# Kernel tuning notes

Hardware: AMD Instinct MI355X
Metric: run time of the kernel (lower is better)

## Reference

```python
import jax, jax.numpy as jnp
import numpy as np

D = 1024

def setup_inputs() -> dict:
    key = jax.random.key(0)
    ks = jax.random.split(key, 9)
    B, S = 4, 2048
    s = 1.0 / np.sqrt(D)
    return {
        "query": jax.random.normal(ks[0], (B, S, D), jnp.float32),
        "key": jax.random.normal(ks[1], (B, S, D), jnp.float32),
        "value": jax.random.normal(ks[2], (B, S, D), jnp.float32),
        "Wq": jax.random.normal(ks[3], (D, D), jnp.float32) * s,
        "bq": jax.random.normal(ks[4], (D,), jnp.float32) * 0.01,
        "Wk": jax.random.normal(ks[5], (D, D), jnp.float32) * s,
        "bk": jax.random.normal(ks[6], (D,), jnp.float32) * 0.01,
        "Wv": jax.random.normal(ks[7], (D, D), jnp.float32) * s,
        "bv": jax.random.normal(ks[8], (D,), jnp.float32) * 0.01,
    }

def reference(query, key, value, Wq, bq, Wk, bk, Wv, bv):
    scale = 1.0 / (query.shape[-1] ** 0.5)
    q = jnp.einsum('bsd,ed->bse', query, Wq) + bq  # nn.Linear: x @ W.T + b
    k = jnp.einsum('bsd,ed->bse', key, Wk) + bk
    v = jnp.einsum('bsd,ed->bse', value, Wv) + bv
    scores = jnp.einsum('bqd,bkd->bqk', q, k) * scale  # [B, Sq, Skv]
    w = jax.nn.softmax(scores, axis=-1)
    return jnp.einsum('bqk,bkd->bqd', w, v)
```

## Files before the change

kernel.cpp:

```cpp
#include <hip/hip_runtime.h>

typedef __bf16 bf16x8 __attribute__((ext_vector_type(8)));
typedef float f32x4 __attribute__((ext_vector_type(4)));
typedef unsigned short u16x8 __attribute__((ext_vector_type(8)));

__device__ inline unsigned short f2bf(float f) {
  union { float f; unsigned u; } a; a.f = f;
  return (unsigned short)((a.u + 0x7fffu + ((a.u >> 16) & 1u)) >> 16);
}
__device__ inline float bf2f(unsigned short h) {
  union { unsigned u; float f; } a; a.u = ((unsigned)h) << 16;
  return a.f;
}

__global__ __launch_bounds__(256) void cvtW(const float* __restrict__ Wq,
                                            const float* __restrict__ Wk,
                                            const float* __restrict__ Wv,
                                            unsigned short* __restrict__ Wb) {
  int i = blockIdx.x * 256 + threadIdx.x;
  int idx = i >> 18;
  int off = i & 262143;
  const float* s = (idx == 0) ? Wq : ((idx == 1) ? Wk : Wv);
  float4 v = ((const float4*)s)[off];
  ushort4 o;
  o.x = f2bf(v.x); o.y = f2bf(v.y); o.z = f2bf(v.z); o.w = f2bf(v.w);
  ((ushort4*)(Wb + idx * 1048576))[off] = o;
}

#define G2L(gp, lp) __builtin_amdgcn_global_load_lds( \
    (const __attribute__((address_space(1))) void*)(gp), \
    (__attribute__((address_space(3))) void*)(lp), 16, 0, 0)

#define MFMA_(d, a, b) d = __builtin_amdgcn_mfma_f32_16x16x32_bf16(a, b, d, 0, 0, 0)
#define SB0() __builtin_amdgcn_sched_barrier(0)
#define LGKM(n) do { asm volatile("s_waitcnt lgkmcnt(" #n ")" ::: "memory"); SB0(); } while (0)
#define VMC(n) do { asm volatile("s_waitcnt vmcnt(" #n ")" ::: "memory"); SB0(); } while (0)

struct PJ {
  const float* A0; const float* A1; const float* A2;
  const unsigned short* B;
  unsigned short* outQ; unsigned short* outK; unsigned short* outV;
  const float* biasQ; const float* biasK; const float* biasV;
};

__global__ __launch_bounds__(512, 2) void gemmP(PJ p) {
  extern __shared__ char smem[];
  char* smA = smem;
  char* smB = smem + 65536;
  const int tid = threadIdx.x, lane = tid & 63, wid = tid >> 6;
  const int wm = wid >> 1, wn = wid & 1;

  int orig = blockIdx.x + 8 * (blockIdx.y + 32 * blockIdx.z);
  int wg = (orig & 7) * 96 + (orig >> 3);
  int bx = wg & 7; int t2 = wg >> 3; int by = t2 & 31; int z = t2 >> 5;
  const int m0 = by << 8, n0 = bx << 7;

  const float* Az = (z == 0) ? p.A0 : ((z == 1) ? p.A1 : p.A2);

  const int lineT = tid >> 3;
  const int sg = (tid & 7) ^ (lineT & 7);
  const char* srcA = (const char*)(Az + (long long)(m0 + lineT) * 1024) + (sg << 4);
  const int srowB = 2 * lineT + (sg >> 2);
  const char* srcB = (const char*)(p.B + (long long)z * 1048576
                                   + (long long)(n0 + srowB) * 1024) + ((sg & 3) << 4);

  const int aBase = (((wm << 6) + (lane & 15)) << 7);
  const int ax = lane & 7;
  const int ck0 = ((((lane >> 4) << 1) | 0) ^ ax) << 4;
  const int ck1 = ((((lane >> 4) << 1) | 1) ^ ax) << 4;
  const int rb2 = (lane & 15) >> 1;
  const int bBase = ((wn << 5) + rb2) << 7;
  const int bX = ((((lane & 1) << 2) | (lane >> 4)) ^ rb2) << 4;

  f32x4 acc[4][4];
#pragma unroll
  for (int i = 0; i < 4; ++i)
#pragma unroll
    for (int j = 0; j < 4; ++j) acc[i][j] = (f32x4){0.f, 0.f, 0.f, 0.f};

  f32x4 aLoF[2][2], aHiF[2][2];
  bf16x8 aLoB[2], aHiB[2], bLo[2], bHi[2];

  auto stage = [&](int t) {
    char* dA = smA + ((t & 1) << 15) + (tid << 4);
    char* dB = smB + ((t & 1) << 13) + (tid << 4);
    const char* sA = srcA + (long long)t * 128;
#pragma unroll
    for (int c = 0; c < 4; ++c) G2L(sA + ((long long)c << 18), dA + (c << 13));
    G2L(srcB + (long long)t * 64, dB);
  };
  auto readA = [&](int b, int half, f32x4 (&dst)[2][2]) {
    const char* ra = smA + (b << 15) + aBase + (half << 12);
#pragma unroll
    for (int f = 0; f < 2; ++f) {
      dst[f][0] = *(const f32x4*)(ra + (f << 11) + ck0);
      dst[f][1] = *(const f32x4*)(ra + (f << 11) + ck1);
    }
  };
  auto readB = [&](int b, int half, bf16x8 (&dst)[2]) {
    const char* rb = smB + (b << 13) + bBase + (half << 11);
#pragma unroll
    for (int f = 0; f < 2; ++f)
      dst[f] = *(const bf16x8*)(rb + (f << 10) + bX);
  };
  auto cvtA = [&](f32x4 (&s)[2][2], bf16x8 (&d)[2]) {
#pragma unroll
    for (int f = 0; f < 2; ++f)
      d[f] = (bf16x8){(__bf16)s[f][0][0], (__bf16)s[f][0][1],
                      (__bf16)s[f][0][2], (__bf16)s[f][0][3],
                      (__bf16)s[f][1][0], (__bf16)s[f][1][1],
                      (__bf16)s[f][1][2], (__bf16)s[f][1][3]};
  };
  auto quadP = [&](int qa, int qb, bf16x8 (&A)[2], bf16x8 (&B)[2]) {
    __builtin_amdgcn_s_setprio(1);
#pragma unroll
    for (int mi = 0; mi < 2; ++mi)
#pragma unroll
      for (int ni = 0; ni < 2; ++ni)
        MFMA_(acc[qa * 2 + mi][qb * 2 + ni], A[mi], B[ni]);
    __builtin_amdgcn_s_setprio(0);
  };

  stage(0);
  VMC(0);
  __builtin_amdgcn_s_barrier();
  readA(0, 0, aLoF); readB(0, 0, bLo);
  SB0();

  const int NT = 32;
  for (int t = 0; t < NT; ++t) {
    if (t + 1 < NT) stage(t + 1);
    SB0();
    LGKM(2);
    cvtA(aLoF, aLoB);
    readA(t & 1, 1, aHiF);
    SB0();
    LGKM(4);
    quadP(0, 0, aLoB, bLo);
    readB(t & 1, 1, bHi);
    SB0();
    LGKM(2);
    cvtA(aHiF, aHiB);
    quadP(1, 0, aHiB, bLo);
    LGKM(0);
    quadP(0, 1, aLoB, bHi);
    quadP(1, 1, aHiB, bHi);
    VMC(0);
    __builtin_amdgcn_s_barrier();
    if (t + 1 < NT) { readA((t + 1) & 1, 0, aLoF); readB((t + 1) & 1, 0, bLo); }
    SB0();
  }

  const int c0 = lane & 15, r0 = (lane >> 4) << 2;
  if (z < 2) {
    unsigned short* O = (z == 0) ? p.outQ : p.outK;
    const float* bias = (z == 0) ? p.biasQ : p.biasK;
#pragma unroll
    for (int mi = 0; mi < 4; ++mi) {
      const int grow = m0 + (wm << 6) + (mi << 4) + r0;
#pragma unroll
      for (int ni = 0; ni < 4; ++ni) {
        const int gcol = n0 + (wn << 6) + (ni << 4) + c0;
        const float bb = bias[gcol];
#pragma unroll
        for (int rr = 0; rr < 4; ++rr)
          O[(long long)(grow + rr) * 1024 + gcol] = f2bf(acc[mi][ni][rr] + bb);
      }
    }
  } else {
#pragma unroll
    for (int mi = 0; mi < 4; ++mi) {
      const int grow = m0 + (wm << 6) + (mi << 4) + r0;
      const int bb = grow >> 11, s = grow & 2047;
#pragma unroll
      for (int ni = 0; ni < 4; ++ni) {
        const int d = n0 + (wn << 6) + (ni << 4) + c0;
        const float ba = p.biasV[d];
        ushort4 pk;
        pk.x = f2bf(acc[mi][ni][0] + ba);
        pk.y = f2bf(acc[mi][ni][1] + ba);
        pk.z = f2bf(acc[mi][ni][2] + ba);
        pk.w = f2bf(acc[mi][ni][3] + ba);
        *(ushort4*)(p.outV + ((long long)bb << 21) + (long long)d * 2048 + s) = pk;
      }
    }
  }
}

#define EPI_SCALE 1
#define EPI_OUT 2

struct GP {
  const unsigned short* A;
  const unsigned short* B;
  unsigned short* C;
  long long batchA, batchB, batchC;
  int lda, ldb, ldc, K;
  float scale;
};

template<int BM, int BN, int WMW, int WNW, int EPI>
__global__ __launch_bounds__(512, 2) void gemm2(GP p) {
  constexpr int NWN = BN / WNW;
  constexpr int AMF = WMW / 16, BNF = WNW / 16;
  constexpr int AH = AMF / 2, BH = BNF / 2;
  constexpr int AF_N = AH * 2;
  constexpr int NBA = BM / 64, NBB = BN / 64;
  static_assert((BM / WMW) * NWN == 8, "8 waves");
  static_assert(BNF == 4, "lgkm immediates assume BNF==4");

  extern __shared__ char smem[];
  char* smA = smem;
  char* smB = smem + 2 * BM * 128;

  const int tid = threadIdx.x;
  const int lane = tid & 63;
  const int wid = tid >> 6;
  const int wm = wid / NWN, wn = wid % NWN;

  const int gx = gridDim.x, gy = gridDim.y;
  const int nwg = gx * gy * (int)gridDim.z;
  int orig = blockIdx.x + gx * (blockIdx.y + gy * blockIdx.z);
  int qq = nwg >> 3, rr_ = nwg & 7;
  int xcd = orig & 7, sl = orig >> 3;
  int wg = (xcd < rr_ ? xcd * (qq + 1) : rr_ * (qq + 1) + (xcd - rr_) * qq) + sl;
  int bx = wg % gx;
  int t2 = wg / gx;
  int by = t2 % gy;
  int z  = t2 / gy;

  const int m0 = by * BM, n0 = bx * BN;

  const long long lda2 = (long long)p.lda * 2;
  const long long ldb2 = (long long)p.ldb * 2;
  const char* Abase = (const char*)(p.A + (long long)z * p.batchA) + (long long)m0 * lda2;
  const char* Bbase = (const char*)(p.B + (long long)z * p.batchB) + (long long)n0 * ldb2;

  const int trow = tid >> 3;
  const int cs = (((tid & 7) ^ (trow & 7)) << 4);
  const char* srcA = Abase + (long long)trow * lda2 + cs;
  const char* srcB = Bbase + (long long)trow * ldb2 + cs;

  const int NT = p.K >> 6;

  const int aRowB = ((wm * WMW + (lane & 15)) << 7);
  const int bRowB = ((wn * WNW + (lane & 15)) << 7);
  const int csw = (lane & 7) << 4;
  const int ck0 = (((lane >> 4) << 4)) ^ csw;
  const int ck1 = ((((lane >> 4) << 4)) | 64) ^ csw;

  f32x4 acc[AMF][BNF];
#pragma unroll
  for (int i = 0; i < AMF; ++i)
#pragma unroll
    for (int j = 0; j < BNF; ++j) acc[i][j] = (f32x4){0.f, 0.f, 0.f, 0.f};

  bf16x8 aLo[AH][2], aHi[AH][2], bLo[BH][2], bHi[BH][2];

  auto stage = [&](int t) {
    char* dA = smA + (t & 1) * (BM * 128) + (tid << 4);
    char* dB = smB + (t & 1) * (BN * 128) + (tid << 4);
    const char* sA = srcA + (long long)t * 128;
    const char* sB = srcB + (long long)t * 128;
#pragma unroll
    for (int c = 0; c < NBA; ++c) G2L(sA + (long long)c * (lda2 << 6), dA + c * 8192);
#pragma unroll
    for (int c = 0; c < NBB; ++c) G2L(sB + (long long)c * (ldb2 << 6), dB + c * 8192);
  };
  auto readAh = [&](int t, int half, bf16x8 (&dst)[AH][2]) {
    const char* ra = smA + (t & 1) * (BM * 128) + aRowB + half * (AH * 2048);
#pragma unroll
    for (int mi = 0; mi < AH; ++mi) {
      dst[mi][0] = *(const bf16x8*)(ra + mi * 2048 + ck0);
      dst[mi][1] = *(const bf16x8*)(ra + mi * 2048 + ck1);
    }
  };
  auto readBh = [&](int t, int half, bf16x8 (&dst)[BH][2]) {
    const char* rb = smB + (t & 1) * (BN * 128) + bRowB + half * (BH * 2048);
#pragma unroll
    for (int ni = 0; ni < BH; ++ni) {
      dst[ni][0] = *(const bf16x8*)(rb + ni * 2048 + ck0);
      dst[ni][1] = *(const bf16x8*)(rb + ni * 2048 + ck1);
    }
  };
  auto quad = [&](int qa, int qb, bf16x8 (&A)[AH][2], bf16x8 (&B)[BH][2]) {
    __builtin_amdgcn_s_setprio(1);
#pragma unroll
    for (int mi = 0; mi < AH; ++mi)
#pragma unroll
      for (int ni = 0; ni < BH; ++ni) {
        MFMA_(acc[qa * AH + mi][qb * BH + ni], A[mi][0], B[ni][0]);
        MFMA_(acc[qa * AH + mi][qb * BH + ni], A[mi][1], B[ni][1]);
      }
    __builtin_amdgcn_s_setprio(0);
  };

  stage(0); stage(1);
  if constexpr (NBA + NBB == 8) VMC(8); else VMC(6);
  __builtin_amdgcn_s_barrier();
  readAh(0, 0, aLo); readBh(0, 0, bLo);
  SB0();

  for (int t = 0; t < NT; ++t) {
    readAh(t, 1, aHi);
    SB0();
    if constexpr (AF_N == 8) LGKM(8); else LGKM(4);
    quad(0, 0, aLo, bLo);
    readBh(t, 1, bHi);
    SB0();
    LGKM(4);
    quad(1, 0, aHi, bLo);
    LGKM(0);
    quad(0, 1, aLo, bHi);
    quad(1, 1, aHi, bHi);
    VMC(0);
    __builtin_amdgcn_s_barrier();
    if (t + 2 < NT) stage(t + 2);
    if (t + 1 < NT) { readAh(t + 1, 0, aLo); readBh(t + 1, 0, bLo); }
    SB0();
  }

  const int c0 = lane & 15;
  const int r0 = (lane >> 4) << 2;
  if constexpr (EPI == EPI_SCALE) {
    unsigned short* Cz = p.C + (long long)z * p.batchC;
#pragma unroll
    for (int mi = 0; mi < AMF; ++mi) {
      const int grow = m0 + wm * WMW + (mi << 4) + r0;
#pragma unroll
      for (int ni = 0; ni < BNF; ++ni) {
        const int gcol = n0 + wn * WNW + (ni << 4) + c0;
#pragma unroll
        for (int rr = 0; rr < 4; ++rr)
          Cz[(long long)(grow + rr) * p.ldc + gcol] = f2bf(acc[mi][ni][rr] * p.scale);
      }
    }
  } else {
    float* Cz = (float*)p.C + (long long)z * p.batchC;
#pragma unroll
    for (int mi = 0; mi < AMF; ++mi) {
      const int grow = m0 + wm * WMW + (mi << 4) + r0;
#pragma unroll
      for (int ni = 0; ni < BNF; ++ni) {
        const int gcol = n0 + wn * WNW + (ni << 4) + c0;
#pragma unroll
        for (int rr = 0; rr < 4; ++rr)
          Cz[(long long)(grow + rr) * p.ldc + gcol] = acc[mi][ni][rr] * p.scale;
      }
    }
  }
}

__global__ __launch_bounds__(256) void softmax_rows(unsigned short* __restrict__ S) {
  const size_t row = blockIdx.x;
  unsigned short* pp = S + row * 2048;
  const int t = threadIdx.x, lane = t & 63, wave = t >> 6;
  u16x8 h = ((const u16x8*)pp)[t];
  float x[8];
#pragma unroll
  for (int j = 0; j < 8; ++j) x[j] = bf2f(h[j]);
  float m = x[0];
#pragma unroll
  for (int j = 1; j < 8; ++j) m = fmaxf(m, x[j]);
#pragma unroll
  for (int off = 32; off >= 1; off >>= 1) m = fmaxf(m, __shfl_xor(m, off, 64));
  __shared__ float rmax[4], rsum[4];
  if (lane == 0) rmax[wave] = m;
  __syncthreads();
  m = fmaxf(fmaxf(rmax[0], rmax[1]), fmaxf(rmax[2], rmax[3]));
  float e[8], sum = 0.f;
#pragma unroll
  for (int j = 0; j < 8; ++j) { e[j] = __expf(x[j] - m); sum += e[j]; }
#pragma unroll
  for (int off = 32; off >= 1; off >>= 1) sum += __shfl_xor(sum, off, 64);
  if (lane == 0) rsum[wave] = sum;
  __syncthreads();
  sum = rsum[0] + rsum[1] + rsum[2] + rsum[3];
  const float inv = 1.f / sum;
  u16x8 o;
#pragma unroll
  for (int j = 0; j < 8; ++j) o[j] = f2bf(e[j] * inv);
  ((u16x8*)pp)[t] = o;
}

extern "C" void kernel_launch(void* const* d_in, const int* in_sizes, int n_in,
                              void* d_out, int out_size, void* d_ws, size_t ws_size,
                              hipStream_t stream) {
  const float* q  = (const float*)d_in[0];
  const float* k  = (const float*)d_in[1];
  const float* v  = (const float*)d_in[2];
  const float* Wq = (const float*)d_in[3];
  const float* bq = (const float*)d_in[4];
  const float* Wk = (const float*)d_in[5];
  const float* bk = (const float*)d_in[6];
  const float* Wv = (const float*)d_in[7];
  const float* bv = (const float*)d_in[8];

  unsigned short* S  = (unsigned short*)d_ws;
  unsigned short* Wb = S + 16777216;
  unsigned short* qb = Wb + 3145728;
  unsigned short* kb = qb + 8388608;
  unsigned short* vT = kb + 8388608;

  (void)hipFuncSetAttribute((const void*)gemmP,
      hipFuncAttributeMaxDynamicSharedMemorySize, 81920);
  (void)hipFuncSetAttribute((const void*)gemm2<256,256,128,64,EPI_SCALE>,
      hipFuncAttributeMaxDynamicSharedMemorySize, 131072);
  (void)hipFuncSetAttribute((const void*)gemm2<256,128,64,64,EPI_OUT>,
      hipFuncAttributeMaxDynamicSharedMemorySize, 98304);

  cvtW<<<3072, 256, 0, stream>>>(Wq, Wk, Wv, Wb);

  PJ pj{};
  pj.A0 = q; pj.A1 = k; pj.A2 = v;
  pj.B = Wb;
  pj.outQ = qb; pj.outK = kb; pj.outV = vT;
  pj.biasQ = bq; pj.biasK = bk; pj.biasV = bv;
  gemmP<<<dim3(8, 32, 3), 512, 81920, stream>>>(pj);

  GP gs{};
  gs.A = qb; gs.batchA = 2097152; gs.lda = 1024;
  gs.B = kb; gs.batchB = 2097152; gs.ldb = 1024;
  gs.C = S;  gs.batchC = 4194304; gs.ldc = 2048;
  gs.K = 1024; gs.scale = 0.03125f;
  gemm2<256,256,128,64,EPI_SCALE><<<dim3(8, 8, 4), 512, 131072, stream>>>(gs);

  softmax_rows<<<8192, 256, 0, stream>>>(S);

  GP gv{};
  gv.A = S;  gv.batchA = 4194304; gv.lda = 2048;
  gv.B = vT; gv.batchB = 2097152; gv.ldb = 2048;
  gv.C = (unsigned short*)d_out; gv.batchC = 2097152; gv.ldc = 1024;
  gv.K = 2048; gv.scale = 1.f;
  gemm2<256,128,64,64,EPI_OUT><<<dim3(8, 8, 4), 512, 98304, stream>>>(gv);
}
```

Baseline: 166.9 us.

## Use 4-wave blocks with 64x128 per-wave tiles in projection GEMM

The QKV projection GEMM now runs with 256 threads (4 waves) instead of 512. Each wave covers a full 64x128 output slab, holding a 4x8 accumulator array instead of 4x4. The global-to-LDS staging, the swizzled LDS read addressing and the wait counts are rewritten to match. The aim is more MFMA work per LDS-loaded B fragment and fewer waves to synchronise, at the cost of higher register pressure and fewer waves to hide latency.

```diff
diff --git a/kernel.cpp b/kernel.cpp
--- a/kernel.cpp
+++ b/kernel.cpp
@@ -43,12 +43,12 @@
   const float* biasQ; const float* biasK; const float* biasV;
 };
 
-__global__ __launch_bounds__(512, 2) void gemmP(PJ p) {
+__global__ __launch_bounds__(256, 2) void gemmP(PJ p) {
   extern __shared__ char smem[];
   char* smA = smem;
   char* smB = smem + 65536;
   const int tid = threadIdx.x, lane = tid & 63, wid = tid >> 6;
-  const int wm = wid >> 1, wn = wid & 1;
+  const int wm = wid;
 
   int orig = blockIdx.x + 8 * (blockIdx.y + 32 * blockIdx.z);
   int wg = (orig & 7) * 96 + (orig >> 3);
@@ -57,51 +57,59 @@
 
   const float* Az = (z == 0) ? p.A0 : ((z == 1) ? p.A1 : p.A2);
 
-  const int lineT = tid >> 3;
-  const int sg = (tid & 7) ^ (lineT & 7);
-  const char* srcA = (const char*)(Az + (long long)(m0 + lineT) * 1024) + (sg << 4);
-  const int srowB = 2 * lineT + (sg >> 2);
-  const char* srcB = (const char*)(p.B + (long long)z * 1048576
-                                   + (long long)(n0 + srowB) * 1024) + ((sg & 3) << 4);
-
-  const int aBase = (((wm << 6) + (lane & 15)) << 7);
-  const int ax = lane & 7;
-  const int ck0 = ((((lane >> 4) << 1) | 0) ^ ax) << 4;
-  const int ck1 = ((((lane >> 4) << 1) | 1) ^ ax) << 4;
-  const int rb2 = (lane & 15) >> 1;
-  const int bBase = ((wn << 5) + rb2) << 7;
-  const int bX = ((((lane & 1) << 2) | (lane >> 4)) ^ rb2) << 4;
-
-  f32x4 acc[4][4];
+  const int sgA = (tid & 7) ^ ((tid >> 3) & 7);
+  const char* srcA = (const char*)Az
+      + ((long long)m0 + 2 * (tid >> 3) + (sgA >> 2)) * 4096 + ((sgA & 3) << 4);
+  const char* srcB = (const char*)(p.B + (long long)z * 1048576)
+      + ((long long)n0 + 2 * (tid >> 3) + (sgA >> 2)) * 2048 + ((sgA & 3) << 4);
+
+  const int kh = lane >> 4;
+  const int Ra0 = (wm << 6) + (lane & 15);
+  const int aJ = (kh >> 1) << 14;
+  const int kq0 = (kh & 1) << 1;
+  const int Rb0 = lane & 15;
+
+  f32x4 acc[4][8];
 #pragma unroll
   for (int i = 0; i < 4; ++i)
 #pragma unroll
-    for (int j = 0; j < 4; ++j) acc[i][j] = (f32x4){0.f, 0.f, 0.f, 0.f};
+    for (int j = 0; j < 8; ++j) acc[i][j] = (f32x4){0.f, 0.f, 0.f, 0.f};
 
   f32x4 aLoF[2][2], aHiF[2][2];
-  bf16x8 aLoB[2], aHiB[2], bLo[2], bHi[2];
+  bf16x8 aLoB[2], aHiB[2], bLo[4], bHi[4];
 
   auto stage = [&](int t) {
     char* dA = smA + ((t & 1) << 15) + (tid << 4);
     char* dB = smB + ((t & 1) << 13) + (tid << 4);
     const char* sA = srcA + (long long)t * 128;
-#pragma unroll
-    for (int c = 0; c < 4; ++c) G2L(sA + ((long long)c << 18), dA + (c << 13));
-    G2L(srcB + (long long)t * 64, dB);
+    const char* sB = srcB + (long long)t * 64;
+#pragma unroll
+    for (int c = 0; c < 8; ++c)
+      G2L(sA + (long long)(c & 3) * 64 * 4096 + ((c >> 2) << 6), dA + (c << 12));
+#pragma unroll
+    for (int c = 0; c < 2; ++c)
+      G2L(sB + (long long)c * 64 * 2048, dB + (c << 12));
   };
   auto readA = [&](int b, int half, f32x4 (&dst)[2][2]) {
-    const char* ra = smA + (b << 15) + aBase + (half << 12);
+    const char* ra = smA + (b << 15) + aJ;
 #pragma unroll
     for (int f = 0; f < 2; ++f) {
-      dst[f][0] = *(const f32x4*)(ra + (f << 11) + ck0);
-      dst[f][1] = *(const f32x4*)(ra + (f << 11) + ck1);
-    }
-  };
-  auto readB = [&](int b, int half, bf16x8 (&dst)[2]) {
-    const char* rb = smB + (b << 13) + bBase + (half << 11);
-#pragma unroll
-    for (int f = 0; f < 2; ++f)
-      dst[f] = *(const bf16x8*)(rb + (f << 10) + bX);
+      const int R = Ra0 + ((half * 2 + f) << 4);
+      const int lineB = (R >> 1) << 7;
+      const int x = ((R & 1) << 2) ^ ((R >> 1) & 7);
+      dst[f][0] = *(const f32x4*)(ra + lineB + ((x ^ (kq0 | 0)) << 4));
+      dst[f][1] = *(const f32x4*)(ra + lineB + ((x ^ (kq0 | 1)) << 4));
+    }
+  };
+  auto readB = [&](int b, int half, bf16x8 (&dst)[4]) {
+    const char* rb = smB + (b << 13);
+#pragma unroll
+    for (int f = 0; f < 4; ++f) {
+      const int R = Rb0 + ((half * 4 + f) << 4);
+      const int byte = ((R >> 1) << 7)
+                     + (((((R & 1) << 2) | kh) ^ ((R >> 1) & 7)) << 4);
+      dst[f] = *(const bf16x8*)(rb + byte);
+    }
   };
   auto cvtA = [&](f32x4 (&s)[2][2], bf16x8 (&d)[2]) {
 #pragma unroll
@@ -111,13 +119,13 @@
                       (__bf16)s[f][1][0], (__bf16)s[f][1][1],
                       (__bf16)s[f][1][2], (__bf16)s[f][1][3]};
   };
-  auto quadP = [&](int qa, int qb, bf16x8 (&A)[2], bf16x8 (&B)[2]) {
+  auto quadP = [&](int qa, int qb, bf16x8 (&A)[2], bf16x8 (&B)[4]) {
     __builtin_amdgcn_s_setprio(1);
 #pragma unroll
     for (int mi = 0; mi < 2; ++mi)
 #pragma unroll
-      for (int ni = 0; ni < 2; ++ni)
-        MFMA_(acc[qa * 2 + mi][qb * 2 + ni], A[mi], B[ni]);
+      for (int ni = 0; ni < 4; ++ni)
+        MFMA_(acc[qa * 2 + mi][qb * 4 + ni], A[mi], B[ni]);
     __builtin_amdgcn_s_setprio(0);
   };
 
@@ -130,16 +138,14 @@
   const int NT = 32;
   for (int t = 0; t < NT; ++t) {
     if (t + 1 < NT) stage(t + 1);
-    SB0();
-    LGKM(2);
+    readA(t & 1, 1, aHiF);
+    SB0();
+    LGKM(4);
     cvtA(aLoF, aLoB);
-    readA(t & 1, 1, aHiF);
-    SB0();
-    LGKM(4);
     quadP(0, 0, aLoB, bLo);
     readB(t & 1, 1, bHi);
     SB0();
-    LGKM(2);
+    LGKM(4);
     cvtA(aHiF, aHiB);
     quadP(1, 0, aHiB, bLo);
     LGKM(0);
@@ -159,8 +165,8 @@
     for (int mi = 0; mi < 4; ++mi) {
       const int grow = m0 + (wm << 6) + (mi << 4) + r0;
 #pragma unroll
-      for (int ni = 0; ni < 4; ++ni) {
-        const int gcol = n0 + (wn << 6) + (ni << 4) + c0;
+      for (int ni = 0; ni < 8; ++ni) {
+        const int gcol = n0 + (ni << 4) + c0;
         const float bb = bias[gcol];
 #pragma unroll
         for (int rr = 0; rr < 4; ++rr)
@@ -173,8 +179,8 @@
       const int grow = m0 + (wm << 6) + (mi << 4) + r0;
       const int bb = grow >> 11, s = grow & 2047;
 #pragma unroll
-      for (int ni = 0; ni < 4; ++ni) {
-        const int d = n0 + (wn << 6) + (ni << 4) + c0;
+      for (int ni = 0; ni < 8; ++ni) {
+        const int d = n0 + (ni << 4) + c0;
         const float ba = p.biasV[d];
         ushort4 pk;
         pk.x = f2bf(acc[mi][ni][0] + ba);
@@ -416,7 +422,7 @@
   pj.B = Wb;
   pj.outQ = qb; pj.outK = kb; pj.outV = vT;
   pj.biasQ = bq; pj.biasK = bk; pj.biasV = bv;
-  gemmP<<<dim3(8, 32, 3), 512, 81920, stream>>>(pj);
+  gemmP<<<dim3(8, 32, 3), 256, 81920, stream>>>(pj);
 
   GP gs{};
   gs.A = qb; gs.batchA = 2097152; gs.lda = 1024;
```

New measurement: 176.7 us. +5.8%, slower.

## Convert projection A operand to bf16 in registers before LDS, shrink tiles

Applied to the files above, without the earlier changes.

The projection GEMM now loads fp32 activations into registers, converts them to bf16, and writes them swizzled into LDS, instead of DMA-ing fp32 straight into LDS and converting after each LDS read. The block tile shrinks from 256x128 with 512 threads to 128x128 with 256 threads, the K step doubles to 128, and LDS use drops to 64KB. The aim is to halve LDS footprint and read bandwidth for A and raise occupancy. The cost is register-staged global loads and VALU conversion inside the main loop, which may overlap less well with the MFMAs.

```diff
diff --git a/kernel.cpp b/kernel.cpp
--- a/kernel.cpp
+++ b/kernel.cpp
@@ -43,34 +43,32 @@
   const float* biasQ; const float* biasK; const float* biasV;
 };
 
-__global__ __launch_bounds__(512, 2) void gemmP(PJ p) {
+__global__ __launch_bounds__(256) void gemmP(PJ p) {
   extern __shared__ char smem[];
   char* smA = smem;
-  char* smB = smem + 65536;
+  char* smB = smem + 32768;
   const int tid = threadIdx.x, lane = tid & 63, wid = tid >> 6;
   const int wm = wid >> 1, wn = wid & 1;
 
-  int orig = blockIdx.x + 8 * (blockIdx.y + 32 * blockIdx.z);
-  int wg = (orig & 7) * 96 + (orig >> 3);
-  int bx = wg & 7; int t2 = wg >> 3; int by = t2 & 31; int z = t2 >> 5;
-  const int m0 = by << 8, n0 = bx << 7;
+  int orig = blockIdx.x + 8 * (blockIdx.y + 64 * blockIdx.z);
+  int wg = (orig & 7) * 192 + (orig >> 3);
+  int bx = wg & 7; int t2 = wg >> 3; int by = t2 & 63; int z = t2 >> 6;
+  const int m0 = by << 7, n0 = bx << 7;
 
   const float* Az = (z == 0) ? p.A0 : ((z == 1) ? p.A1 : p.A2);
 
-  const int lineT = tid >> 3;
-  const int sg = (tid & 7) ^ (lineT & 7);
-  const char* srcA = (const char*)(Az + (long long)(m0 + lineT) * 1024) + (sg << 4);
-  const int srowB = 2 * lineT + (sg >> 2);
+  const char* srcA0 = (const char*)Az + ((long long)m0 + (tid >> 4)) * 4096
+                    + ((tid & 15) << 4);
+  const int trow = tid >> 3;
+  const int cs = (((tid & 7) ^ (trow & 7)) << 4);
   const char* srcB = (const char*)(p.B + (long long)z * 1048576
-                                   + (long long)(n0 + srowB) * 1024) + ((sg & 3) << 4);
-
-  const int aBase = (((wm << 6) + (lane & 15)) << 7);
-  const int ax = lane & 7;
-  const int ck0 = ((((lane >> 4) << 1) | 0) ^ ax) << 4;
-  const int ck1 = ((((lane >> 4) << 1) | 1) ^ ax) << 4;
-  const int rb2 = (lane & 15) >> 1;
-  const int bBase = ((wn << 5) + rb2) << 7;
-  const int bX = ((((lane & 1) << 2) | (lane >> 4)) ^ rb2) << 4;
+                                   + (long long)(n0 + trow) * 1024) + cs;
+
+  const int aRowB = (((wm << 6) + (lane & 15)) << 7);
+  const int bRowB = (((wn << 6) + (lane & 15)) << 7);
+  const int csw = (lane & 7) << 4;
+  const int ck0 = (((lane >> 4) << 4)) ^ csw;
+  const int ck1 = ((((lane >> 4) << 4)) | 64) ^ csw;
 
   f32x4 acc[4][4];
 #pragma unroll
@@ -78,76 +76,97 @@
 #pragma unroll
     for (int j = 0; j < 4; ++j) acc[i][j] = (f32x4){0.f, 0.f, 0.f, 0.f};
 
-  f32x4 aLoF[2][2], aHiF[2][2];
-  bf16x8 aLoB[2], aHiB[2], bLo[2], bHi[2];
-
-  auto stage = [&](int t) {
-    char* dA = smA + ((t & 1) << 15) + (tid << 4);
-    char* dB = smB + ((t & 1) << 13) + (tid << 4);
-    const char* sA = srcA + (long long)t * 128;
-#pragma unroll
-    for (int c = 0; c < 4; ++c) G2L(sA + ((long long)c << 18), dA + (c << 13));
-    G2L(srcB + (long long)t * 64, dB);
-  };
-  auto readA = [&](int b, int half, f32x4 (&dst)[2][2]) {
-    const char* ra = smA + (b << 15) + aBase + (half << 12);
-#pragma unroll
-    for (int f = 0; f < 2; ++f) {
-      dst[f][0] = *(const f32x4*)(ra + (f << 11) + ck0);
-      dst[f][1] = *(const f32x4*)(ra + (f << 11) + ck1);
-    }
-  };
-  auto readB = [&](int b, int half, bf16x8 (&dst)[2]) {
-    const char* rb = smB + (b << 13) + bBase + (half << 11);
-#pragma unroll
-    for (int f = 0; f < 2; ++f)
-      dst[f] = *(const bf16x8*)(rb + (f << 10) + bX);
-  };
-  auto cvtA = [&](f32x4 (&s)[2][2], bf16x8 (&d)[2]) {
-#pragma unroll
-    for (int f = 0; f < 2; ++f)
-      d[f] = (bf16x8){(__bf16)s[f][0][0], (__bf16)s[f][0][1],
-                      (__bf16)s[f][0][2], (__bf16)s[f][0][3],
-                      (__bf16)s[f][1][0], (__bf16)s[f][1][1],
-                      (__bf16)s[f][1][2], (__bf16)s[f][1][3]};
-  };
-  auto quadP = [&](int qa, int qb, bf16x8 (&A)[2], bf16x8 (&B)[2]) {
+  float4 areg[8];
+  bf16x8 aLo[2][2], aHi[2][2], bLo[2][2], bHi[2][2];
+
+  auto ldA = [&](int t) {
+    const char* s = srcA0 + (long long)t * 256;
+#pragma unroll
+    for (int c = 0; c < 8; ++c)
+      areg[c] = *(const float4*)(s + (long long)c * 65536);
+  };
+  auto wrA = [&](int t) {
+    char* dA = smA + ((t & 1) << 14);
+    const int g = (tid & 15) >> 1;
+    const int hb = (tid & 1) << 3;
+#pragma unroll
+    for (int c = 0; c < 8; ++c) {
+      const int rc = (c << 4) + (tid >> 4);
+      float4 v = areg[c];
+      ushort4 o;
+      o.x = f2bf(v.x); o.y = f2bf(v.y); o.z = f2bf(v.z); o.w = f2bf(v.w);
+      *(ushort4*)(dA + (rc << 7) + ((g ^ (rc & 7)) << 4) + hb) = o;
+    }
+  };
+  auto stageB = [&](int t) {
+    char* dB = smB + ((t & 1) << 14) + (tid << 4);
+    const char* sB = srcB + (long long)t * 128;
+#pragma unroll
+    for (int c = 0; c < 4; ++c)
+      G2L(sB + (long long)c * 65536, dB + (c << 12));
+  };
+  auto readAh = [&](int b, int half, bf16x8 (&dst)[2][2]) {
+    const char* ra = smA + (b << 14) + aRowB + (half << 12);
+#pragma unroll
+    for (int mi = 0; mi < 2; ++mi) {
+      dst[mi][0] = *(const bf16x8*)(ra + (mi << 11) + ck0);
+      dst[mi][1] = *(const bf16x8*)(ra + (mi << 11) + ck1);
+    }
+  };
+  auto readBh = [&](int b, int half, bf16x8 (&dst)[2][2]) {
+    const char* rb = smB + (b << 14) + bRowB + (half << 12);
+#pragma unroll
+    for (int ni = 0; ni < 2; ++ni) {
+      dst[ni][0] = *(const bf16x8*)(rb + (ni << 11) + ck0);
+      dst[ni][1] = *(const bf16x8*)(rb + (ni << 11) + ck1);
+    }
+  };
+  auto quad = [&](int qa, int qb, bf16x8 (&A)[2][2], bf16x8 (&B)[2][2]) {
     __builtin_amdgcn_s_setprio(1);
 #pragma unroll
     for (int mi = 0; mi < 2; ++mi)
 #pragma unroll
-      for (int ni = 0; ni < 2; ++ni)
-        MFMA_(acc[qa * 2 + mi][qb * 2 + ni], A[mi], B[ni]);
+      for (int ni = 0; ni < 2; ++ni) {
+        MFMA_(acc[qa * 2 + mi][qb * 2 + ni], A[mi][0], B[ni][0]);
+        MFMA_(acc[qa * 2 + mi][qb * 2 + ni], A[mi][1], B[ni][1]);
+      }
     __builtin_amdgcn_s_setprio(0);
   };
 
-  stage(0);
+  ldA(0); stageB(0);
+  VMC(4);
+  wrA(0);
   VMC(0);
+  LGKM(0);
   __builtin_amdgcn_s_barrier();
-  readA(0, 0, aLoF); readB(0, 0, bLo);
+  readAh(0, 0, aLo); readBh(0, 0, bLo);
   SB0();
 
-  const int NT = 32;
+  const int NT = 16;
   for (int t = 0; t < NT; ++t) {
-    if (t + 1 < NT) stage(t + 1);
-    SB0();
-    LGKM(2);
-    cvtA(aLoF, aLoB);
-    readA(t & 1, 1, aHiF);
+    const bool pf = (t + 1) < NT;
+    if (pf) { ldA(t + 1); stageB(t + 1); }
+    readAh(t & 1, 1, aHi);
     SB0();
     LGKM(4);
-    quadP(0, 0, aLoB, bLo);
-    readB(t & 1, 1, bHi);
-    SB0();
-    LGKM(2);
-    cvtA(aHiF, aHiB);
-    quadP(1, 0, aHiB, bLo);
+    quad(0, 0, aLo, bLo);
+    readBh(t & 1, 1, bHi);
+    SB0();
+    LGKM(4);
+    quad(1, 0, aHi, bLo);
     LGKM(0);
-    quadP(0, 1, aLoB, bHi);
-    quadP(1, 1, aHiB, bHi);
-    VMC(0);
+    quad(0, 1, aLo, bHi);
+    quad(1, 1, aHi, bHi);
+    if (pf) {
+      VMC(4);
+      wrA(t + 1);
+      VMC(0);
+    } else {
+      VMC(0);
+    }
+    LGKM(0);
     __builtin_amdgcn_s_barrier();
-    if (t + 1 < NT) { readA((t + 1) & 1, 0, aLoF); readB((t + 1) & 1, 0, bLo); }
+    if (pf) { readAh((t + 1) & 1, 0, aLo); readBh((t + 1) & 1, 0, bLo); }
     SB0();
   }
 
@@ -403,7 +422,7 @@
   unsigned short* vT = kb + 8388608;
 
   (void)hipFuncSetAttribute((const void*)gemmP,
-      hipFuncAttributeMaxDynamicSharedMemorySize, 81920);
+      hipFuncAttributeMaxDynamicSharedMemorySize, 65536);
   (void)hipFuncSetAttribute((const void*)gemm2<256,256,128,64,EPI_SCALE>,
       hipFuncAttributeMaxDynamicSharedMemorySize, 131072);
   (void)hipFuncSetAttribute((const void*)gemm2<256,128,64,64,EPI_OUT>,
@@ -416,7 +435,7 @@
   pj.B = Wb;
   pj.outQ = qb; pj.outK = kb; pj.outV = vT;
   pj.biasQ = bq; pj.biasK = bk; pj.biasV = bv;
-  gemmP<<<dim3(8, 32, 3), 512, 81920, stream>>>(pj);
+  gemmP<<<dim3(8, 64, 3), 256, 65536, stream>>>(pj);
 
   GP gs{};
   gs.A = qb; gs.batchA = 2097152; gs.lda = 1024;
```

New measurement: 174.5 us. 1.05x slower.
